# Optimization experiments

Measured on AMD Instinct MI355X. Metric: run time of the kernel, lower is better.

## Reference

```python
import jax, jax.numpy as jnp
import numpy as np

N_NODES = 50000
N_EDGES = 1600000
IN_FEATS = 256
OUT_FEATS = 64


def setup_inputs() -> dict:
    key = jax.random.key(0)
    k_x, k_w, k_b, k_s, k_d = jax.random.split(key, 5)
    x = jax.random.normal(k_x, (N_NODES, IN_FEATS), dtype=jnp.float32)
    # nn.Linear(in_feats, out_feats): weight [out, in], bias [out]
    W = jax.random.normal(k_w, (OUT_FEATS, IN_FEATS), dtype=jnp.float32) / np.sqrt(IN_FEATS)
    b = jax.random.normal(k_b, (OUT_FEATS,), dtype=jnp.float32) * 0.01
    edge_src = jax.random.randint(k_s, (N_EDGES,), 0, N_NODES, dtype=jnp.int32)
    edge_dst = jax.random.randint(k_d, (N_EDGES,), 0, N_NODES, dtype=jnp.int32)
    return {"x": x, "W": W, "b": b, "edge_src": edge_src, "edge_dst": edge_dst}


def reference(x, W, b, edge_src, edge_dst):
    # h = dropout(relu(Linear(x)))  -- dropout p=0 (eval) => identity
    h = jax.nn.relu(x @ W.T + b)                     # [N, out_feats]
    # update_all: message = h[src], reduce = mean over incoming edges per dst
    msg = h[edge_src]                                # [E, out_feats] gather
    summed = jax.ops.segment_sum(msg, edge_dst, num_segments=N_NODES)  # [N, out]
    deg = jax.ops.segment_sum(jnp.ones((edge_src.shape[0],), dtype=h.dtype),
                              edge_dst, num_segments=N_NODES)          # [N]
    deg = jnp.maximum(deg, 1.0)
    return summed / deg[:, None]
```

## Files before the change

kernel.cpp:

```cpp
#include <hip/hip_runtime.h>
#include <hip/hip_bf16.h>

#define K_IN 256
#define O_OUT 64
#define NBINS 1024
#define NPB 49
#define CAP 1824
#define PART_CHUNK 4096

typedef __attribute__((ext_vector_type(8))) short short8;
typedef __attribute__((ext_vector_type(4))) float f32x4;

__device__ inline unsigned short bf16bits(float a) {
  __hip_bfloat16 t = __float2bfloat16(a);
  return *(unsigned short*)&t;
}

__device__ inline short8 cvt8(float4 f0, float4 f1) {
  short8 r;
  r[0] = (short)bf16bits(f0.x); r[1] = (short)bf16bits(f0.y);
  r[2] = (short)bf16bits(f0.z); r[3] = (short)bf16bits(f0.w);
  r[4] = (short)bf16bits(f1.x); r[5] = (short)bf16bits(f1.y);
  r[6] = (short)bf16bits(f1.z); r[7] = (short)bf16bits(f1.w);
  return r;
}

__global__ __launch_bounds__(256) void k_prep(const float* __restrict__ W,
                                              unsigned short* __restrict__ Wb,
                                              int* __restrict__ cursor) {
  int i = blockIdx.x * 256 + threadIdx.x;
  Wb[i] = bf16bits(W[i]);
  if (i < NBINS) cursor[i] = 0;
}

struct GemmSmem {
  unsigned short wsb[64 * 256];
};
struct PartSmem {
  int cnt[NBINS];
  int scanb[NBINS];
  int gbase[NBINS];
  int wsum[4];
  unsigned ord[PART_CHUNK];
};
union FusedSmem {
  GemmSmem g;
  PartSmem p;
};

__device__ void gemm_body(GemmSmem& sm, int gid, const float* __restrict__ x,
                          const unsigned short* __restrict__ Wb,
                          const float* __restrict__ bias,
                          __hip_bfloat16* __restrict__ h, int N) {
  const int tid = threadIdx.x;
  const int lane = tid & 63;
  const int wv = tid >> 6;

  {
    const uint4* wsrc = (const uint4*)Wb;
    uint4 wtmp[8];
#pragma unroll
    for (int r = 0; r < 8; ++r) wtmp[r] = wsrc[r * 256 + tid];
    __builtin_amdgcn_sched_barrier(0);
#pragma unroll
    for (int r = 0; r < 8; ++r) {
      int flat = r * 256 + tid;
      int row = flat >> 5;
      int c16 = flat & 31;
      unsigned byte = (unsigned)(row * 512 + c16 * 16);
      byte ^= (unsigned)((row & 7) << 4);
      *(uint4*)((char*)sm.wsb + byte) = wtmp[r];
    }
  }
  __syncthreads();

  const int brow0 = lane & 15;
  const unsigned kb = (unsigned)((lane >> 4) * 16);
  const unsigned bswz = (unsigned)((brow0 & 7) << 4);

#pragma unroll
  for (int t = 0; t < 2; ++t) {
    const int n0 = gid * 128 + t * 64;
    int anode = n0 + wv * 16 + (lane & 15);
    if (anode > N - 1) anode = N - 1;
    const float* aptr = x + (size_t)anode * K_IN + (lane >> 4) * 8;

    float4 f[16];
#pragma unroll
    for (int k8 = 0; k8 < 8; ++k8) {
      f[2 * k8] = *(const float4*)(aptr + k8 * 32);
      f[2 * k8 + 1] = *(const float4*)(aptr + k8 * 32 + 4);
    }
    __builtin_amdgcn_sched_barrier(0);

    f32x4 acc[4] = {{0.f, 0.f, 0.f, 0.f}, {0.f, 0.f, 0.f, 0.f},
                    {0.f, 0.f, 0.f, 0.f}, {0.f, 0.f, 0.f, 0.f}};
#pragma unroll
    for (int k8 = 0; k8 < 8; ++k8) {
      short8 a = cvt8(f[2 * k8], f[2 * k8 + 1]);
#pragma unroll
      for (int nt = 0; nt < 4; ++nt) {
        unsigned byte = (unsigned)((brow0 + nt * 16) * 512 + k8 * 64) + kb;
        byte ^= bswz;
        short8 bfr = *(const short8*)((const char*)sm.wsb + byte);
        acc[nt] = __builtin_amdgcn_mfma_f32_16x16x32_bf16(a, bfr, acc[nt], 0, 0, 0);
      }
    }

    const int col = lane & 15;
    const int rbase = (lane >> 4) * 4;
#pragma unroll
    for (int nt = 0; nt < 4; ++nt) {
      float bv = bias[nt * 16 + col];
#pragma unroll
      for (int j = 0; j < 4; ++j) {
        int node = n0 + wv * 16 + rbase + j;
        if (node < N) {
          float v = fmaxf(acc[nt][j] + bv, 0.f);
          h[(size_t)node * O_OUT + nt * 16 + col] = __float2bfloat16(v);
        }
      }
    }
  }
}

__device__ void part_body(PartSmem& sm, int pid, const int* __restrict__ esrc,
                          const int* __restrict__ edst, int* __restrict__ cursor,
                          unsigned* __restrict__ bucket, int E) {
  const int tid = threadIdx.x;
  const int lane = tid & 63;
  const int wid = tid >> 6;
  const int base = pid * PART_CHUNK;

#pragma unroll
  for (int r = 0; r < 4; ++r) sm.cnt[r * 256 + tid] = 0;

  int4 s4[4], d4[4];
#pragma unroll
  for (int r = 0; r < 4; ++r) {
    int e0 = base + r * 1024 + tid * 4;
    if (e0 + 3 < E) {
      s4[r] = *(const int4*)(esrc + e0);
      d4[r] = *(const int4*)(edst + e0);
    } else {
      s4[r] = make_int4(0, 0, 0, 0);
      d4[r] = make_int4(0, 0, 0, 0);
      int* sp = (int*)&s4[r];
      int* dp = (int*)&d4[r];
      for (int j = 0; j < 4; ++j)
        if (e0 + j < E) { sp[j] = esrc[e0 + j]; dp[j] = edst[e0 + j]; }
    }
  }
  __builtin_amdgcn_sched_barrier(0);
  __syncthreads();

  unsigned pk[16];
  int rk[16];
#pragma unroll
  for (int r = 0; r < 4; ++r) {
    const int* sp = (const int*)&s4[r];
    const int* dp = (const int*)&d4[r];
#pragma unroll
    for (int j = 0; j < 4; ++j) {
      int k = r * 4 + j;
      int e = base + r * 1024 + tid * 4 + j;
      if (e < E) {
        int d = dp[j];
        int bb = (int)__umulhi((unsigned)d, 87652394u);
        int dl = d - bb * NPB;
        pk[k] = (unsigned)sp[j] | ((unsigned)dl << 16) | ((unsigned)bb << 22);
        rk[k] = atomicAdd(&sm.cnt[bb], 1);
      } else {
        rk[k] = -1;
      }
    }
  }
  __syncthreads();

  int c0 = sm.cnt[4 * tid];
  int c1 = sm.cnt[4 * tid + 1];
  int c2 = sm.cnt[4 * tid + 2];
  int c3 = sm.cnt[4 * tid + 3];
  int s = c0 + c1 + c2 + c3;
  int incl = s;
#pragma unroll
  for (int off = 1; off < 64; off <<= 1) {
    int t = __shfl_up(incl, off);
    if (lane >= off) incl += t;
  }
  if (lane == 63) sm.wsum[wid] = incl;
  __syncthreads();
  int wpre = 0;
  for (int w = 0; w < wid; ++w) wpre += sm.wsum[w];
  int excl = wpre + incl - s;
  sm.scanb[4 * tid] = excl;
  sm.scanb[4 * tid + 1] = excl + c0;
  sm.scanb[4 * tid + 2] = excl + c0 + c1;
  sm.scanb[4 * tid + 3] = excl + c0 + c1 + c2;
  sm.gbase[4 * tid] = (c0 > 0) ? atomicAdd(&cursor[4 * tid], c0) : 0;
  sm.gbase[4 * tid + 1] = (c1 > 0) ? atomicAdd(&cursor[4 * tid + 1], c1) : 0;
  sm.gbase[4 * tid + 2] = (c2 > 0) ? atomicAdd(&cursor[4 * tid + 2], c2) : 0;
  sm.gbase[4 * tid + 3] = (c3 > 0) ? atomicAdd(&cursor[4 * tid + 3], c3) : 0;
  __syncthreads();

#pragma unroll
  for (int k = 0; k < 16; ++k) {
    if (rk[k] >= 0) {
      int bb = (int)(pk[k] >> 22);
      int pos = sm.scanb[bb] + rk[k];
      sm.ord[pos] = pk[k];
    }
  }
  __syncthreads();

  int nv = E - base;
  if (nv > PART_CHUNK) nv = PART_CHUNK;
  for (int p = tid; p < nv; p += 256) {
    unsigned v = sm.ord[p];
    int bb = v >> 22;
    int slot = sm.gbase[bb] + (p - sm.scanb[bb]);
    if (slot < CAP) bucket[(size_t)bb * CAP + slot] = v;
  }
}

__global__ __launch_bounds__(256, 4) void k_fused(const float* __restrict__ x,
                                                  const unsigned short* __restrict__ Wb,
                                                  const float* __restrict__ bias,
                                                  __hip_bfloat16* __restrict__ h,
                                                  const int* __restrict__ esrc,
                                                  const int* __restrict__ edst,
                                                  int* __restrict__ cursor,
                                                  unsigned* __restrict__ bucket,
                                                  int N, int E) {
  __shared__ FusedSmem sm;
  const int ngemm2 = (N + 127) / 128;
  const int npart = (E + PART_CHUNK - 1) / PART_CHUNK;
  const int m2 = ngemm2 < npart ? ngemm2 : npart;
  const int b = blockIdx.x;
  if (b < 2 * m2) {
    if (b & 1) part_body(sm.p, b >> 1, esrc, edst, cursor, bucket, E);
    else gemm_body(sm.g, b >> 1, x, Wb, bias, h, N);
  } else {
    int idx = b - m2;
    if (ngemm2 > npart) gemm_body(sm.g, idx, x, Wb, bias, h, N);
    else part_body(sm.p, idx, esrc, edst, cursor, bucket, E);
  }
}

__global__ __launch_bounds__(256, 4) void k_sortagg(const unsigned* __restrict__ bucket,
                                                    const int* __restrict__ cursor,
                                                    const unsigned* __restrict__ h32,
                                                    float* __restrict__ out, int N) {
  __shared__ int hist[NPB];
  __shared__ int offs[NPB];
  __shared__ unsigned short sbuf[CAP + 64];

  const int tid = threadIdx.x;
  const int lane = tid & 63;
  const int wid = tid >> 6;
  const int bin = blockIdx.x;

  if (tid < NPB) hist[tid] = 0;
  __syncthreads();

  int cnt = cursor[bin];
  if (cnt > CAP) cnt = CAP;
  const unsigned* bb = bucket + (size_t)bin * CAP;

  unsigned pk2[2][4];
  int rk2[2][4];
#pragma unroll
  for (int g = 0; g < 2; ++g) {
    int i0 = (g * 256 + tid) * 4;
    uint4 v;
    if (i0 + 3 < cnt) {
      v = *(const uint4*)(bb + i0);
    } else {
      v = make_uint4(0, 0, 0, 0);
      unsigned* vp = (unsigned*)&v;
      for (int j = 0; j < 4; ++j)
        if (i0 + j < cnt) vp[j] = bb[i0 + j];
    }
    const unsigned* vp = (const unsigned*)&v;
#pragma unroll
    for (int j = 0; j < 4; ++j) {
      if (i0 + j < cnt) {
        pk2[g][j] = vp[j];
        rk2[g][j] = atomicAdd(&hist[(vp[j] >> 16) & 63], 1);
      } else {
        rk2[g][j] = -1;
      }
    }
  }
  __syncthreads();

  if (tid < 64) {
    int hval = (tid < NPB) ? hist[tid] : 0;
    int incl = hval;
#pragma unroll
    for (int off = 1; off < 64; off <<= 1) {
      int t = __shfl_up(incl, off);
      if (lane >= off) incl += t;
    }
    if (tid < NPB) offs[tid] = incl - hval;
  }
  __syncthreads();

#pragma unroll
  for (int g = 0; g < 2; ++g)
#pragma unroll
    for (int j = 0; j < 4; ++j)
      if (rk2[g][j] >= 0)
        sbuf[offs[(pk2[g][j] >> 16) & 63] + rk2[g][j]] =
            (unsigned short)(pk2[g][j] & 0xFFFFu);
  __syncthreads();

  const int q = lane >> 4;
  const int hl = lane & 15;
  const uint2* __restrict__ h2 = (const uint2*)h32;

  for (int nl = wid; nl < NPB; nl += 8) {
    const int nlb = nl + 4;
    const bool hasb = (nlb < NPB);
    const int ca = hist[nl];
    const int cb = hasb ? hist[nlb] : 0;
    const unsigned short* bsa = sbuf + offs[nl];
    const unsigned short* bsb = sbuf + (hasb ? offs[nlb] : 0);

    int pa[12], pb[12];
#pragma unroll
    for (int k = 0; k < 12; ++k) {
      int e = k * 4 + q;
      pa[k] = (e < ca) ? (int)bsa[e] : 0;
      pb[k] = (e < cb) ? (int)bsb[e] : 0;
    }
    uint2 ua[12], ub[12];
#pragma unroll
    for (int k = 0; k < 12; ++k) ua[k] = h2[(size_t)pa[k] * 16 + hl];
#pragma unroll
    for (int k = 0; k < 12; ++k) ub[k] = h2[(size_t)pb[k] * 16 + hl];
    __builtin_amdgcn_sched_barrier(0);

    float a0 = 0.f, a1 = 0.f, a2 = 0.f, a3 = 0.f;
    float b0 = 0.f, b1 = 0.f, b2 = 0.f, b3 = 0.f;
#pragma unroll
    for (int k = 0; k < 12; ++k) {
      float wk = (k * 4 + q < ca) ? 1.f : 0.f;
      a0 = fmaf(wk, __uint_as_float(ua[k].x << 16), a0);
      a1 = fmaf(wk, __uint_as_float(ua[k].x & 0xFFFF0000u), a1);
      a2 = fmaf(wk, __uint_as_float(ua[k].y << 16), a2);
      a3 = fmaf(wk, __uint_as_float(ua[k].y & 0xFFFF0000u), a3);
    }
#pragma unroll
    for (int k = 0; k < 12; ++k) {
      float wk = (k * 4 + q < cb) ? 1.f : 0.f;
      b0 = fmaf(wk, __uint_as_float(ub[k].x << 16), b0);
      b1 = fmaf(wk, __uint_as_float(ub[k].x & 0xFFFF0000u), b1);
      b2 = fmaf(wk, __uint_as_float(ub[k].y << 16), b2);
      b3 = fmaf(wk, __uint_as_float(ub[k].y & 0xFFFF0000u), b3);
    }

    for (int e0 = 48; e0 < ca; e0 += 4) {
      int e = e0 + q;
      float wk = (e < ca) ? 1.f : 0.f;
      int p = (e < ca) ? (int)bsa[e] : 0;
      uint2 u = h2[(size_t)p * 16 + hl];
      a0 = fmaf(wk, __uint_as_float(u.x << 16), a0);
      a1 = fmaf(wk, __uint_as_float(u.x & 0xFFFF0000u), a1);
      a2 = fmaf(wk, __uint_as_float(u.y << 16), a2);
      a3 = fmaf(wk, __uint_as_float(u.y & 0xFFFF0000u), a3);
    }
    for (int e0 = 48; e0 < cb; e0 += 4) {
      int e = e0 + q;
      float wk = (e < cb) ? 1.f : 0.f;
      int p = (e < cb) ? (int)bsb[e] : 0;
      uint2 u = h2[(size_t)p * 16 + hl];
      b0 = fmaf(wk, __uint_as_float(u.x << 16), b0);
      b1 = fmaf(wk, __uint_as_float(u.x & 0xFFFF0000u), b1);
      b2 = fmaf(wk, __uint_as_float(u.y << 16), b2);
      b3 = fmaf(wk, __uint_as_float(u.y & 0xFFFF0000u), b3);
    }

    a0 += __shfl_xor(a0, 16); a1 += __shfl_xor(a1, 16);
    a2 += __shfl_xor(a2, 16); a3 += __shfl_xor(a3, 16);
    b0 += __shfl_xor(b0, 16); b1 += __shfl_xor(b1, 16);
    b2 += __shfl_xor(b2, 16); b3 += __shfl_xor(b3, 16);
    a0 += __shfl_xor(a0, 32); a1 += __shfl_xor(a1, 32);
    a2 += __shfl_xor(a2, 32); a3 += __shfl_xor(a3, 32);
    b0 += __shfl_xor(b0, 32); b1 += __shfl_xor(b1, 32);
    b2 += __shfl_xor(b2, 32); b3 += __shfl_xor(b3, 32);

    if (lane < 16) {
      int na = bin * NPB + nl;
      if (na < N) {
        float inv = 1.f / fmaxf((float)ca, 1.f);
        float4 r;
        r.x = a0 * inv; r.y = a1 * inv; r.z = a2 * inv; r.w = a3 * inv;
        *(float4*)(out + (size_t)na * O_OUT + hl * 4) = r;
      }
      int nb = bin * NPB + nlb;
      if (hasb && nb < N) {
        float inv = 1.f / fmaxf((float)cb, 1.f);
        float4 r;
        r.x = b0 * inv; r.y = b1 * inv; r.z = b2 * inv; r.w = b3 * inv;
        *(float4*)(out + (size_t)nb * O_OUT + hl * 4) = r;
      }
    }
  }
}

extern "C" void kernel_launch(void* const* d_in, const int* in_sizes, int n_in,
                              void* d_out, int out_size, void* d_ws, size_t ws_size,
                              hipStream_t stream) {
  const float* x = (const float*)d_in[0];
  const float* W = (const float*)d_in[1];
  const float* b = (const float*)d_in[2];
  const int* esrc = (const int*)d_in[3];
  const int* edst = (const int*)d_in[4];
  float* out = (float*)d_out;

  const int N = in_sizes[0] / K_IN;
  const int E = in_sizes[3];

  char* ws = (char*)d_ws;
  unsigned short* Wb = (unsigned short*)ws;
  __hip_bfloat16* h = (__hip_bfloat16*)(ws + 32768);
  size_t off = 32768 + (size_t)N * O_OUT * sizeof(__hip_bfloat16);
  int* cursor = (int*)(ws + off);
  off += NBINS * sizeof(int);
  unsigned* bucket = (unsigned*)(ws + off);

  const int ngemm2 = (N + 127) / 128;
  const int npart = (E + PART_CHUNK - 1) / PART_CHUNK;

  k_prep<<<(K_IN * O_OUT) / 256, 256, 0, stream>>>(W, Wb, cursor);
  k_fused<<<ngemm2 + npart, 256, 0, stream>>>(x, Wb, b, h, esrc, edst, cursor,
                                              bucket, N, E);
  k_sortagg<<<NBINS, 256, 0, stream>>>(bucket, cursor, (const unsigned*)h, out, N);
}
```

Measured before the change: 163.0 us.

## Split fused GEMM/partition kernel into separate launches with 64-row GEMM tiles

Replaces the interleaved fused kernel, which mixed GEMM and edge-partition blocks through a shared-memory union, with two separate kernels, k_part and k_gemm, launched back to back. The GEMM now handles 64 rows per block instead of 128, doubling the block count. It also issues the x-row loads before the barrier that follows the W staging into LDS. The split gives each kernel its own LDS footprint and register allocation, at the cost of an extra launch and no overlap between the partition and GEMM work.

```diff
diff --git a/kernel.cpp b/kernel.cpp
--- a/kernel.cpp
+++ b/kernel.cpp
@@ -33,28 +33,16 @@
   if (i < NBINS) cursor[i] = 0;
 }
 
-struct GemmSmem {
-  unsigned short wsb[64 * 256];
-};
-struct PartSmem {
-  int cnt[NBINS];
-  int scanb[NBINS];
-  int gbase[NBINS];
-  int wsum[4];
-  unsigned ord[PART_CHUNK];
-};
-union FusedSmem {
-  GemmSmem g;
-  PartSmem p;
-};
-
-__device__ void gemm_body(GemmSmem& sm, int gid, const float* __restrict__ x,
-                          const unsigned short* __restrict__ Wb,
-                          const float* __restrict__ bias,
-                          __hip_bfloat16* __restrict__ h, int N) {
+__global__ __launch_bounds__(256, 4) void k_gemm(const float* __restrict__ x,
+                                                 const unsigned short* __restrict__ Wb,
+                                                 const float* __restrict__ bias,
+                                                 __hip_bfloat16* __restrict__ h,
+                                                 int N) {
+  __shared__ unsigned short wsb[64 * 256];
   const int tid = threadIdx.x;
   const int lane = tid & 63;
   const int wv = tid >> 6;
+  const int n0 = blockIdx.x * 64;
 
   {
     const uint4* wsrc = (const uint4*)Wb;
@@ -69,8 +57,19 @@
       int c16 = flat & 31;
       unsigned byte = (unsigned)(row * 512 + c16 * 16);
       byte ^= (unsigned)((row & 7) << 4);
-      *(uint4*)((char*)sm.wsb + byte) = wtmp[r];
-    }
+      *(uint4*)((char*)wsb + byte) = wtmp[r];
+    }
+  }
+
+  int anode = n0 + wv * 16 + (lane & 15);
+  if (anode > N - 1) anode = N - 1;
+  const float* aptr = x + (size_t)anode * K_IN + (lane >> 4) * 8;
+
+  float4 f[16];
+#pragma unroll
+  for (int k8 = 0; k8 < 8; ++k8) {
+    f[2 * k8] = *(const float4*)(aptr + k8 * 32);
+    f[2 * k8 + 1] = *(const float4*)(aptr + k8 * 32 + 4);
   }
   __syncthreads();
 
@@ -78,62 +77,54 @@
   const unsigned kb = (unsigned)((lane >> 4) * 16);
   const unsigned bswz = (unsigned)((brow0 & 7) << 4);
 
-#pragma unroll
-  for (int t = 0; t < 2; ++t) {
-    const int n0 = gid * 128 + t * 64;
-    int anode = n0 + wv * 16 + (lane & 15);
-    if (anode > N - 1) anode = N - 1;
-    const float* aptr = x + (size_t)anode * K_IN + (lane >> 4) * 8;
-
-    float4 f[16];
-#pragma unroll
-    for (int k8 = 0; k8 < 8; ++k8) {
-      f[2 * k8] = *(const float4*)(aptr + k8 * 32);
-      f[2 * k8 + 1] = *(const float4*)(aptr + k8 * 32 + 4);
-    }
-    __builtin_amdgcn_sched_barrier(0);
-
-    f32x4 acc[4] = {{0.f, 0.f, 0.f, 0.f}, {0.f, 0.f, 0.f, 0.f},
-                    {0.f, 0.f, 0.f, 0.f}, {0.f, 0.f, 0.f, 0.f}};
-#pragma unroll
-    for (int k8 = 0; k8 < 8; ++k8) {
-      short8 a = cvt8(f[2 * k8], f[2 * k8 + 1]);
-#pragma unroll
-      for (int nt = 0; nt < 4; ++nt) {
-        unsigned byte = (unsigned)((brow0 + nt * 16) * 512 + k8 * 64) + kb;
-        byte ^= bswz;
-        short8 bfr = *(const short8*)((const char*)sm.wsb + byte);
-        acc[nt] = __builtin_amdgcn_mfma_f32_16x16x32_bf16(a, bfr, acc[nt], 0, 0, 0);
+  f32x4 acc[4] = {{0.f, 0.f, 0.f, 0.f}, {0.f, 0.f, 0.f, 0.f},
+                  {0.f, 0.f, 0.f, 0.f}, {0.f, 0.f, 0.f, 0.f}};
+#pragma unroll
+  for (int k8 = 0; k8 < 8; ++k8) {
+    short8 a = cvt8(f[2 * k8], f[2 * k8 + 1]);
+#pragma unroll
+    for (int nt = 0; nt < 4; ++nt) {
+      unsigned byte = (unsigned)((brow0 + nt * 16) * 512 + k8 * 64) + kb;
+      byte ^= bswz;
+      short8 bfr = *(const short8*)((const char*)wsb + byte);
+      acc[nt] = __builtin_amdgcn_mfma_f32_16x16x32_bf16(a, bfr, acc[nt], 0, 0, 0);
+    }
+  }
+
+  const int col = lane & 15;
+  const int rbase = (lane >> 4) * 4;
+#pragma unroll
+  for (int nt = 0; nt < 4; ++nt) {
+    float bv = bias[nt * 16 + col];
+#pragma unroll
+    for (int j = 0; j < 4; ++j) {
+      int node = n0 + wv * 16 + rbase + j;
+      if (node < N) {
+        float v = fmaxf(acc[nt][j] + bv, 0.f);
+        h[(size_t)node * O_OUT + nt * 16 + col] = __float2bfloat16(v);
       }
     }
-
-    const int col = lane & 15;
-    const int rbase = (lane >> 4) * 4;
-#pragma unroll
-    for (int nt = 0; nt < 4; ++nt) {
-      float bv = bias[nt * 16 + col];
-#pragma unroll
-      for (int j = 0; j < 4; ++j) {
-        int node = n0 + wv * 16 + rbase + j;
-        if (node < N) {
-          float v = fmaxf(acc[nt][j] + bv, 0.f);
-          h[(size_t)node * O_OUT + nt * 16 + col] = __float2bfloat16(v);
-        }
-      }
-    }
-  }
-}
-
-__device__ void part_body(PartSmem& sm, int pid, const int* __restrict__ esrc,
-                          const int* __restrict__ edst, int* __restrict__ cursor,
-                          unsigned* __restrict__ bucket, int E) {
+  }
+}
+
+__global__ __launch_bounds__(256, 4) void k_part(const int* __restrict__ esrc,
+                                                 const int* __restrict__ edst,
+                                                 int* __restrict__ cursor,
+                                                 unsigned* __restrict__ bucket,
+                                                 int E) {
+  __shared__ int cnt[NBINS];
+  __shared__ int scanb[NBINS];
+  __shared__ int gbase[NBINS];
+  __shared__ int wsum[4];
+  __shared__ unsigned ord[PART_CHUNK];
+
   const int tid = threadIdx.x;
   const int lane = tid & 63;
   const int wid = tid >> 6;
-  const int base = pid * PART_CHUNK;
-
-#pragma unroll
-  for (int r = 0; r < 4; ++r) sm.cnt[r * 256 + tid] = 0;
+  const int base = blockIdx.x * PART_CHUNK;
+
+#pragma unroll
+  for (int r = 0; r < 4; ++r) cnt[r * 256 + tid] = 0;
 
   int4 s4[4], d4[4];
 #pragma unroll
@@ -169,7 +160,7 @@
         int bb = (int)__umulhi((unsigned)d, 87652394u);
         int dl = d - bb * NPB;
         pk[k] = (unsigned)sp[j] | ((unsigned)dl << 16) | ((unsigned)bb << 22);
-        rk[k] = atomicAdd(&sm.cnt[bb], 1);
+        rk[k] = atomicAdd(&cnt[bb], 1);
       } else {
         rk[k] = -1;
       }
@@ -177,10 +168,10 @@
   }
   __syncthreads();
 
-  int c0 = sm.cnt[4 * tid];
-  int c1 = sm.cnt[4 * tid + 1];
-  int c2 = sm.cnt[4 * tid + 2];
-  int c3 = sm.cnt[4 * tid + 3];
+  int c0 = cnt[4 * tid];
+  int c1 = cnt[4 * tid + 1];
+  int c2 = cnt[4 * tid + 2];
+  int c3 = cnt[4 * tid + 3];
   int s = c0 + c1 + c2 + c3;
   int incl = s;
 #pragma unroll
@@ -188,27 +179,27 @@
     int t = __shfl_up(incl, off);
     if (lane >= off) incl += t;
   }
-  if (lane == 63) sm.wsum[wid] = incl;
+  if (lane == 63) wsum[wid] = incl;
   __syncthreads();
   int wpre = 0;
-  for (int w = 0; w < wid; ++w) wpre += sm.wsum[w];
+  for (int w = 0; w < wid; ++w) wpre += wsum[w];
   int excl = wpre + incl - s;
-  sm.scanb[4 * tid] = excl;
-  sm.scanb[4 * tid + 1] = excl + c0;
-  sm.scanb[4 * tid + 2] = excl + c0 + c1;
-  sm.scanb[4 * tid + 3] = excl + c0 + c1 + c2;
-  sm.gbase[4 * tid] = (c0 > 0) ? atomicAdd(&cursor[4 * tid], c0) : 0;
-  sm.gbase[4 * tid + 1] = (c1 > 0) ? atomicAdd(&cursor[4 * tid + 1], c1) : 0;
-  sm.gbase[4 * tid + 2] = (c2 > 0) ? atomicAdd(&cursor[4 * tid + 2], c2) : 0;
-  sm.gbase[4 * tid + 3] = (c3 > 0) ? atomicAdd(&cursor[4 * tid + 3], c3) : 0;
+  scanb[4 * tid] = excl;
+  scanb[4 * tid + 1] = excl + c0;
+  scanb[4 * tid + 2] = excl + c0 + c1;
+  scanb[4 * tid + 3] = excl + c0 + c1 + c2;
+  gbase[4 * tid] = (c0 > 0) ? atomicAdd(&cursor[4 * tid], c0) : 0;
+  gbase[4 * tid + 1] = (c1 > 0) ? atomicAdd(&cursor[4 * tid + 1], c1) : 0;
+  gbase[4 * tid + 2] = (c2 > 0) ? atomicAdd(&cursor[4 * tid + 2], c2) : 0;
+  gbase[4 * tid + 3] = (c3 > 0) ? atomicAdd(&cursor[4 * tid + 3], c3) : 0;
   __syncthreads();
 
 #pragma unroll
   for (int k = 0; k < 16; ++k) {
     if (rk[k] >= 0) {
       int bb = (int)(pk[k] >> 22);
-      int pos = sm.scanb[bb] + rk[k];
-      sm.ord[pos] = pk[k];
+      int pos = scanb[bb] + rk[k];
+      ord[pos] = pk[k];
     }
   }
   __syncthreads();
@@ -216,34 +207,10 @@
   int nv = E - base;
   if (nv > PART_CHUNK) nv = PART_CHUNK;
   for (int p = tid; p < nv; p += 256) {
-    unsigned v = sm.ord[p];
+    unsigned v = ord[p];
     int bb = v >> 22;
-    int slot = sm.gbase[bb] + (p - sm.scanb[bb]);
+    int slot = gbase[bb] + (p - scanb[bb]);
     if (slot < CAP) bucket[(size_t)bb * CAP + slot] = v;
-  }
-}
-
-__global__ __launch_bounds__(256, 4) void k_fused(const float* __restrict__ x,
-                                                  const unsigned short* __restrict__ Wb,
-                                                  const float* __restrict__ bias,
-                                                  __hip_bfloat16* __restrict__ h,
-                                                  const int* __restrict__ esrc,
-                                                  const int* __restrict__ edst,
-                                                  int* __restrict__ cursor,
-                                                  unsigned* __restrict__ bucket,
-                                                  int N, int E) {
-  __shared__ FusedSmem sm;
-  const int ngemm2 = (N + 127) / 128;
-  const int npart = (E + PART_CHUNK - 1) / PART_CHUNK;
-  const int m2 = ngemm2 < npart ? ngemm2 : npart;
-  const int b = blockIdx.x;
-  if (b < 2 * m2) {
-    if (b & 1) part_body(sm.p, b >> 1, esrc, edst, cursor, bucket, E);
-    else gemm_body(sm.g, b >> 1, x, Wb, bias, h, N);
-  } else {
-    int idx = b - m2;
-    if (ngemm2 > npart) gemm_body(sm.g, idx, x, Wb, bias, h, N);
-    else part_body(sm.p, idx, esrc, edst, cursor, bucket, E);
   }
 }
 
@@ -430,11 +397,11 @@
   off += NBINS * sizeof(int);
   unsigned* bucket = (unsigned*)(ws + off);
 
-  const int ngemm2 = (N + 127) / 128;
+  const int ngemm = (N + 63) / 64;
   const int npart = (E + PART_CHUNK - 1) / PART_CHUNK;
 
   k_prep<<<(K_IN * O_OUT) / 256, 256, 0, stream>>>(W, Wb, cursor);
-  k_fused<<<ngemm2 + npart, 256, 0, stream>>>(x, Wb, b, h, esrc, edst, cursor,
-                                              bucket, N, E);
+  k_part<<<npart, 256, 0, stream>>>(esrc, edst, cursor, bucket, E);
+  k_gemm<<<ngemm, 256, 0, stream>>>(x, Wb, b, h, N);
   k_sortagg<<<NBINS, 256, 0, stream>>>(bucket, cursor, (const unsigned*)h, out, N);
 }
```

New measurement: 172.0 us. +5.5%, slower.

## Issue global loads via inline asm early and rebalance fused gemm/partition blocks

Applied to the files above, without the earlier changes.

The GEMM body now handles 64 nodes per block instead of 128. It issues its x loads with inline-asm global_load_dwordx4 before staging W into LDS, so the global latency overlaps the LDS fill. The partition body issues edge loads before zeroing counters and clamps tail offsets instead of branching. The fused kernel interleaves one partition block per three blocks in place of alternating, and the aggregation gathers use asm loads with a single explicit vmcnt wait. The changes also mask src to 16 bits when packing (src is 0–49999, so this looks lossless) and double the GEMM block count, which risks reloading W into LDS more often.

```diff
diff --git a/kernel.cpp b/kernel.cpp
--- a/kernel.cpp
+++ b/kernel.cpp
@@ -10,18 +10,35 @@
 
 typedef __attribute__((ext_vector_type(8))) short short8;
 typedef __attribute__((ext_vector_type(4))) float f32x4;
+typedef __attribute__((ext_vector_type(2))) unsigned u32x2;
+typedef __attribute__((ext_vector_type(4))) unsigned u32x4;
+
+#define GLOAD4(dst, base, voff, imm)                                     \
+  asm volatile("global_load_dwordx4 %0, %1, %2 offset:" #imm             \
+               : "=v"(dst) : "v"(voff), "s"(base))
+#define GLOAD2(dst, base, voff)                                          \
+  asm volatile("global_load_dwordx2 %0, %1, %2"                          \
+               : "=v"(dst) : "v"(voff), "s"(base))
+__device__ inline void vmwait0() {
+  asm volatile("s_waitcnt vmcnt(0)" ::: "memory");
+  __builtin_amdgcn_sched_barrier(0);
+}
 
 __device__ inline unsigned short bf16bits(float a) {
   __hip_bfloat16 t = __float2bfloat16(a);
   return *(unsigned short*)&t;
 }
 
-__device__ inline short8 cvt8(float4 f0, float4 f1) {
+__device__ inline short8 cvt8u(u32x4 lo, u32x4 hi) {
   short8 r;
-  r[0] = (short)bf16bits(f0.x); r[1] = (short)bf16bits(f0.y);
-  r[2] = (short)bf16bits(f0.z); r[3] = (short)bf16bits(f0.w);
-  r[4] = (short)bf16bits(f1.x); r[5] = (short)bf16bits(f1.y);
-  r[6] = (short)bf16bits(f1.z); r[7] = (short)bf16bits(f1.w);
+  r[0] = (short)bf16bits(__uint_as_float(lo[0]));
+  r[1] = (short)bf16bits(__uint_as_float(lo[1]));
+  r[2] = (short)bf16bits(__uint_as_float(lo[2]));
+  r[3] = (short)bf16bits(__uint_as_float(lo[3]));
+  r[4] = (short)bf16bits(__uint_as_float(hi[0]));
+  r[5] = (short)bf16bits(__uint_as_float(hi[1]));
+  r[6] = (short)bf16bits(__uint_as_float(hi[2]));
+  r[7] = (short)bf16bits(__uint_as_float(hi[3]));
   return r;
 }
 
@@ -55,70 +72,68 @@
   const int tid = threadIdx.x;
   const int lane = tid & 63;
   const int wv = tid >> 6;
+  const int n0 = gid * 64;
+
+  int anode = n0 + wv * 16 + (lane & 15);
+  if (anode > N - 1) anode = N - 1;
+  unsigned voff = (unsigned)anode * (K_IN * 4) + (unsigned)((lane >> 4) * 32);
+
+  u32x4 f[16];
+  GLOAD4(f[0], x, voff, 0);    GLOAD4(f[1], x, voff, 16);
+  GLOAD4(f[2], x, voff, 128);  GLOAD4(f[3], x, voff, 144);
+  GLOAD4(f[4], x, voff, 256);  GLOAD4(f[5], x, voff, 272);
+  GLOAD4(f[6], x, voff, 384);  GLOAD4(f[7], x, voff, 400);
+  GLOAD4(f[8], x, voff, 512);  GLOAD4(f[9], x, voff, 528);
+  GLOAD4(f[10], x, voff, 640); GLOAD4(f[11], x, voff, 656);
+  GLOAD4(f[12], x, voff, 768); GLOAD4(f[13], x, voff, 784);
+  GLOAD4(f[14], x, voff, 896); GLOAD4(f[15], x, voff, 912);
+  __builtin_amdgcn_sched_barrier(0);
 
   {
     const uint4* wsrc = (const uint4*)Wb;
-    uint4 wtmp[8];
-#pragma unroll
-    for (int r = 0; r < 8; ++r) wtmp[r] = wsrc[r * 256 + tid];
-    __builtin_amdgcn_sched_barrier(0);
 #pragma unroll
     for (int r = 0; r < 8; ++r) {
+      uint4 w = wsrc[r * 256 + tid];
       int flat = r * 256 + tid;
       int row = flat >> 5;
       int c16 = flat & 31;
       unsigned byte = (unsigned)(row * 512 + c16 * 16);
       byte ^= (unsigned)((row & 7) << 4);
-      *(uint4*)((char*)sm.wsb + byte) = wtmp[r];
-    }
-  }
-  __syncthreads();
+      *(uint4*)((char*)sm.wsb + byte) = w;
+    }
+  }
+  __syncthreads();
+  vmwait0();
 
   const int brow0 = lane & 15;
   const unsigned kb = (unsigned)((lane >> 4) * 16);
   const unsigned bswz = (unsigned)((brow0 & 7) << 4);
 
-#pragma unroll
-  for (int t = 0; t < 2; ++t) {
-    const int n0 = gid * 128 + t * 64;
-    int anode = n0 + wv * 16 + (lane & 15);
-    if (anode > N - 1) anode = N - 1;
-    const float* aptr = x + (size_t)anode * K_IN + (lane >> 4) * 8;
-
-    float4 f[16];
-#pragma unroll
-    for (int k8 = 0; k8 < 8; ++k8) {
-      f[2 * k8] = *(const float4*)(aptr + k8 * 32);
-      f[2 * k8 + 1] = *(const float4*)(aptr + k8 * 32 + 4);
-    }
-    __builtin_amdgcn_sched_barrier(0);
-
-    f32x4 acc[4] = {{0.f, 0.f, 0.f, 0.f}, {0.f, 0.f, 0.f, 0.f},
-                    {0.f, 0.f, 0.f, 0.f}, {0.f, 0.f, 0.f, 0.f}};
-#pragma unroll
-    for (int k8 = 0; k8 < 8; ++k8) {
-      short8 a = cvt8(f[2 * k8], f[2 * k8 + 1]);
-#pragma unroll
-      for (int nt = 0; nt < 4; ++nt) {
-        unsigned byte = (unsigned)((brow0 + nt * 16) * 512 + k8 * 64) + kb;
-        byte ^= bswz;
-        short8 bfr = *(const short8*)((const char*)sm.wsb + byte);
-        acc[nt] = __builtin_amdgcn_mfma_f32_16x16x32_bf16(a, bfr, acc[nt], 0, 0, 0);
-      }
-    }
-
-    const int col = lane & 15;
-    const int rbase = (lane >> 4) * 4;
+  f32x4 acc[4] = {{0.f, 0.f, 0.f, 0.f}, {0.f, 0.f, 0.f, 0.f},
+                  {0.f, 0.f, 0.f, 0.f}, {0.f, 0.f, 0.f, 0.f}};
+#pragma unroll
+  for (int k8 = 0; k8 < 8; ++k8) {
+    short8 a = cvt8u(f[2 * k8], f[2 * k8 + 1]);
 #pragma unroll
     for (int nt = 0; nt < 4; ++nt) {
-      float bv = bias[nt * 16 + col];
-#pragma unroll
-      for (int j = 0; j < 4; ++j) {
-        int node = n0 + wv * 16 + rbase + j;
-        if (node < N) {
-          float v = fmaxf(acc[nt][j] + bv, 0.f);
-          h[(size_t)node * O_OUT + nt * 16 + col] = __float2bfloat16(v);
-        }
+      unsigned byte = (unsigned)((brow0 + nt * 16) * 512 + k8 * 64) + kb;
+      byte ^= bswz;
+      short8 bfr = *(const short8*)((const char*)sm.wsb + byte);
+      acc[nt] = __builtin_amdgcn_mfma_f32_16x16x32_bf16(a, bfr, acc[nt], 0, 0, 0);
+    }
+  }
+
+  const int col = lane & 15;
+  const int rbase = (lane >> 4) * 4;
+#pragma unroll
+  for (int nt = 0; nt < 4; ++nt) {
+    float bv = bias[nt * 16 + col];
+#pragma unroll
+    for (int j = 0; j < 4; ++j) {
+      int node = n0 + wv * 16 + rbase + j;
+      if (node < N) {
+        float v = fmaxf(acc[nt][j] + bv, 0.f);
+        h[(size_t)node * O_OUT + nt * 16 + col] = __float2bfloat16(v);
       }
     }
   }
@@ -132,43 +147,38 @@
   const int wid = tid >> 6;
   const int base = pid * PART_CHUNK;
 
-#pragma unroll
-  for (int r = 0; r < 4; ++r) sm.cnt[r * 256 + tid] = 0;
-
-  int4 s4[4], d4[4];
+  u32x4 s4[4], d4[4];
+  unsigned vo[4];
 #pragma unroll
   for (int r = 0; r < 4; ++r) {
     int e0 = base + r * 1024 + tid * 4;
-    if (e0 + 3 < E) {
-      s4[r] = *(const int4*)(esrc + e0);
-      d4[r] = *(const int4*)(edst + e0);
-    } else {
-      s4[r] = make_int4(0, 0, 0, 0);
-      d4[r] = make_int4(0, 0, 0, 0);
-      int* sp = (int*)&s4[r];
-      int* dp = (int*)&d4[r];
-      for (int j = 0; j < 4; ++j)
-        if (e0 + j < E) { sp[j] = esrc[e0 + j]; dp[j] = edst[e0 + j]; }
-    }
-  }
+    if (e0 > E - 4) e0 = E - 4;
+    vo[r] = (unsigned)e0 * 4u;
+  }
+  GLOAD4(s4[0], esrc, vo[0], 0); GLOAD4(d4[0], edst, vo[0], 0);
+  GLOAD4(s4[1], esrc, vo[1], 0); GLOAD4(d4[1], edst, vo[1], 0);
+  GLOAD4(s4[2], esrc, vo[2], 0); GLOAD4(d4[2], edst, vo[2], 0);
+  GLOAD4(s4[3], esrc, vo[3], 0); GLOAD4(d4[3], edst, vo[3], 0);
   __builtin_amdgcn_sched_barrier(0);
-  __syncthreads();
+
+#pragma unroll
+  for (int r = 0; r < 4; ++r) sm.cnt[r * 256 + tid] = 0;
+  __syncthreads();
+  vmwait0();
 
   unsigned pk[16];
   int rk[16];
 #pragma unroll
   for (int r = 0; r < 4; ++r) {
-    const int* sp = (const int*)&s4[r];
-    const int* dp = (const int*)&d4[r];
 #pragma unroll
     for (int j = 0; j < 4; ++j) {
       int k = r * 4 + j;
       int e = base + r * 1024 + tid * 4 + j;
       if (e < E) {
-        int d = dp[j];
+        int d = (int)d4[r][j];
         int bb = (int)__umulhi((unsigned)d, 87652394u);
         int dl = d - bb * NPB;
-        pk[k] = (unsigned)sp[j] | ((unsigned)dl << 16) | ((unsigned)bb << 22);
+        pk[k] = (s4[r][j] & 0xFFFFu) | ((unsigned)dl << 16) | ((unsigned)bb << 22);
         rk[k] = atomicAdd(&sm.cnt[bb], 1);
       } else {
         rk[k] = -1;
@@ -233,17 +243,14 @@
                                                   unsigned* __restrict__ bucket,
                                                   int N, int E) {
   __shared__ FusedSmem sm;
-  const int ngemm2 = (N + 127) / 128;
   const int npart = (E + PART_CHUNK - 1) / PART_CHUNK;
-  const int m2 = ngemm2 < npart ? ngemm2 : npart;
   const int b = blockIdx.x;
-  if (b < 2 * m2) {
-    if (b & 1) part_body(sm.p, b >> 1, esrc, edst, cursor, bucket, E);
-    else gemm_body(sm.g, b >> 1, x, Wb, bias, h, N);
+  if (b % 3 == 1 && b / 3 < npart) {
+    part_body(sm.p, b / 3, esrc, edst, cursor, bucket, E);
   } else {
-    int idx = b - m2;
-    if (ngemm2 > npart) gemm_body(sm.g, idx, x, Wb, bias, h, N);
-    else part_body(sm.p, idx, esrc, edst, cursor, bucket, E);
+    int skipped = (b + 2) / 3;
+    if (skipped > npart) skipped = npart;
+    gemm_body(sm.g, b - skipped, x, Wb, bias, h, N);
   }
 }
 
@@ -317,7 +324,7 @@
 
   const int q = lane >> 4;
   const int hl = lane & 15;
-  const uint2* __restrict__ h2 = (const uint2*)h32;
+  const unsigned hlb = (unsigned)hl * 8u;
 
   for (int nl = wid; nl < NPB; nl += 8) {
     const int nlb = nl + 4;
@@ -327,39 +334,42 @@
     const unsigned short* bsa = sbuf + offs[nl];
     const unsigned short* bsb = sbuf + (hasb ? offs[nlb] : 0);
 
-    int pa[12], pb[12];
+    unsigned voa[12], vob[12];
 #pragma unroll
     for (int k = 0; k < 12; ++k) {
       int e = k * 4 + q;
-      pa[k] = (e < ca) ? (int)bsa[e] : 0;
-      pb[k] = (e < cb) ? (int)bsb[e] : 0;
-    }
-    uint2 ua[12], ub[12];
-#pragma unroll
-    for (int k = 0; k < 12; ++k) ua[k] = h2[(size_t)pa[k] * 16 + hl];
-#pragma unroll
-    for (int k = 0; k < 12; ++k) ub[k] = h2[(size_t)pb[k] * 16 + hl];
-    __builtin_amdgcn_sched_barrier(0);
+      unsigned pa = (e < ca) ? (unsigned)bsa[e] : 0u;
+      unsigned pb = (e < cb) ? (unsigned)bsb[e] : 0u;
+      voa[k] = pa * 128u + hlb;
+      vob[k] = pb * 128u + hlb;
+    }
+    u32x2 ua[12], ub[12];
+#pragma unroll
+    for (int k = 0; k < 12; ++k) { GLOAD2(ua[k], h32, voa[k]); }
+#pragma unroll
+    for (int k = 0; k < 12; ++k) { GLOAD2(ub[k], h32, vob[k]); }
+    vmwait0();
 
     float a0 = 0.f, a1 = 0.f, a2 = 0.f, a3 = 0.f;
     float b0 = 0.f, b1 = 0.f, b2 = 0.f, b3 = 0.f;
 #pragma unroll
     for (int k = 0; k < 12; ++k) {
       float wk = (k * 4 + q < ca) ? 1.f : 0.f;
-      a0 = fmaf(wk, __uint_as_float(ua[k].x << 16), a0);
-      a1 = fmaf(wk, __uint_as_float(ua[k].x & 0xFFFF0000u), a1);
-      a2 = fmaf(wk, __uint_as_float(ua[k].y << 16), a2);
-      a3 = fmaf(wk, __uint_as_float(ua[k].y & 0xFFFF0000u), a3);
+      a0 = fmaf(wk, __uint_as_float(ua[k][0] << 16), a0);
+      a1 = fmaf(wk, __uint_as_float(ua[k][0] & 0xFFFF0000u), a1);
+      a2 = fmaf(wk, __uint_as_float(ua[k][1] << 16), a2);
+      a3 = fmaf(wk, __uint_as_float(ua[k][1] & 0xFFFF0000u), a3);
     }
 #pragma unroll
     for (int k = 0; k < 12; ++k) {
       float wk = (k * 4 + q < cb) ? 1.f : 0.f;
-      b0 = fmaf(wk, __uint_as_float(ub[k].x << 16), b0);
-      b1 = fmaf(wk, __uint_as_float(ub[k].x & 0xFFFF0000u), b1);
-      b2 = fmaf(wk, __uint_as_float(ub[k].y << 16), b2);
-      b3 = fmaf(wk, __uint_as_float(ub[k].y & 0xFFFF0000u), b3);
-    }
-
+      b0 = fmaf(wk, __uint_as_float(ub[k][0] << 16), b0);
+      b1 = fmaf(wk, __uint_as_float(ub[k][0] & 0xFFFF0000u), b1);
+      b2 = fmaf(wk, __uint_as_float(ub[k][1] << 16), b2);
+      b3 = fmaf(wk, __uint_as_float(ub[k][1] & 0xFFFF0000u), b3);
+    }
+
+    const uint2* __restrict__ h2 = (const uint2*)h32;
     for (int e0 = 48; e0 < ca; e0 += 4) {
       int e = e0 + q;
       float wk = (e < ca) ? 1.f : 0.f;
@@ -430,11 +440,11 @@
   off += NBINS * sizeof(int);
   unsigned* bucket = (unsigned*)(ws + off);
 
-  const int ngemm2 = (N + 127) / 128;
+  const int ngemm = (N + 63) / 64;
   const int npart = (E + PART_CHUNK - 1) / PART_CHUNK;
 
   k_prep<<<(K_IN * O_OUT) / 256, 256, 0, stream>>>(W, Wb, cursor);
-  k_fused<<<ngemm2 + npart, 256, 0, stream>>>(x, Wb, b, h, esrc, edst, cursor,
-                                              bucket, N, E);
+  k_fused<<<ngemm + npart, 256, 0, stream>>>(x, Wb, b, h, esrc, edst, cursor,
+                                             bucket, N, E);
   k_sortagg<<<NBINS, 256, 0, stream>>>(bucket, cursor, (const unsigned*)h, out, N);
 }
```

After: 160.7 us. Within noise of the previous version (-1.4%).
